# Kernel tuning notes

Hardware: AMD Instinct MI355X
Metric: run time of the kernel (lower is better)

Reference implementation:

```python
import jax, jax.numpy as jnp
import numpy as np

# mamba-370m-style dims (n_layers reduced for tractable reference execution)
H = 1024      # hidden_size
DI = 2048     # intermediate (expand*H)
DS = 16       # ssm state size
DTR = 64      # time_step_rank = H/16
NL = 4        # layers
V = 50280     # vocab after resize_token_embeddings
LLM = 4096    # llm_input_size
B, L = 4, 1024
MEM_ID = 50279
STRIDE = 64
K = L // STRIDE  # mem tokens per sequence
EPS = 1e-5


def setup_inputs() -> dict:
    key = jax.random.key(0)
    ks = jax.random.split(key, 10)
    s = 0.02
    ids = jax.random.randint(ks[0], (B, L), 0, MEM_ID)
    ids = ids.at[:, STRIDE - 1::STRIDE].set(MEM_ID)  # K mem tokens per row
    return {
        "input_ids": ids,
        "embed": jax.random.normal(ks[1], (V, H)) * s,
        "norm_w": jnp.ones((NL, H)),
        "in_proj_w": jax.random.normal(ks[2], (NL, 2 * DI, H)) * s,
        "conv_w": jax.random.normal(ks[3], (NL, DI, 4)) * s,
        "conv_b": jnp.zeros((NL, DI)),
        "x_proj_w": jax.random.normal(ks[4], (NL, DTR + 2 * DS, DI)) * s,
        "dt_w": jax.random.normal(ks[5], (NL, DI, DTR)) * s,
        "dt_b": jax.random.uniform(ks[6], (NL, DI), minval=-4.0, maxval=-2.0),
        "A_log": jnp.log(jnp.broadcast_to(jnp.arange(1, DS + 1, dtype=jnp.float32), (NL, DI, DS))),
        "D": jnp.ones((NL, DI)),
        "out_proj_w": jax.random.normal(ks[7], (NL, H, DI)) * s,
        "final_norm_w": jnp.ones((H,)),
        "proj_w": jax.random.normal(ks[8], (LLM, H)) * s,
        "proj_b": jnp.zeros((LLM,)),
    }


def rmsnorm(x, w):
    return x * jax.lax.rsqrt(jnp.mean(x * x, axis=-1, keepdims=True) + EPS) * w


def mamba_layer(h, p):
    norm_w, in_w, cw, cb, xw, dtw, dtb, A_log, Dp, ow = p
    x = rmsnorm(h, norm_w)
    xz = jnp.einsum('blh,dh->bld', x, in_w)          # (B,L,2*DI)
    x, z = jnp.split(xz, 2, axis=-1)
    # causal depthwise conv1d, kernel 4, left pad 3
    xt = jnp.transpose(x, (0, 2, 1))                  # (B,DI,L)
    xc = jax.lax.conv_general_dilated(xt, cw[:, None, :], (1,), [(3, 0)],
                                      feature_group_count=DI)
    u = jax.nn.silu(xc + cb[None, :, None])
    u = jnp.transpose(u, (0, 2, 1))                   # (B,L,DI)
    ssm = jnp.einsum('bld,ed->ble', u, xw)            # (B,L,DTR+2*DS)
    dt_raw = ssm[..., :DTR]
    Bm = ssm[..., DTR:DTR + DS]
    Cm = ssm[..., DTR + DS:]
    dt = jax.nn.softplus(jnp.einsum('blr,dr->bld', dt_raw, dtw) + dtb)  # (B,L,DI)
    A = -jnp.exp(A_log)                               # (DI,DS)

    def step(s, inp):
        dt_t, B_t, C_t, u_t = inp                     # (B,DI),(B,DS),(B,DS),(B,DI)
        dA = jnp.exp(dt_t[..., None] * A)             # (B,DI,DS)
        s = s * dA + (dt_t * u_t)[..., None] * B_t[:, None, :]
        return s, jnp.einsum('bds,bs->bd', s, C_t)

    s0 = jnp.zeros((h.shape[0], DI, DS), dtype=h.dtype)
    _, ys = jax.lax.scan(step, s0, (dt.swapaxes(0, 1), Bm.swapaxes(0, 1),
                                    Cm.swapaxes(0, 1), u.swapaxes(0, 1)))
    y = ys.swapaxes(0, 1) + u * Dp
    y = y * jax.nn.silu(z)
    return h + jnp.einsum('bld,hd->blh', y, ow), None


def reference(input_ids, embed, norm_w, in_proj_w, conv_w, conv_b, x_proj_w,
              dt_w, dt_b, A_log, D, out_proj_w, final_norm_w, proj_w, proj_b):
    h = embed[input_ids]                              # (B,L,H)
    h, _ = jax.lax.scan(mamba_layer, h,
                        (norm_w, in_proj_w, conv_w, conv_b, x_proj_w,
                         dt_w, dt_b, A_log, D, out_proj_w))
    h = rmsnorm(h, final_norm_w)
    # gather mem-token positions (K per row, in order); stable argsort puts mask hits first
    mask = input_ids == MEM_ID
    pos = jnp.argsort(jnp.where(mask, 0, 1), axis=1)[:, :K]
    feats = jnp.take_along_axis(h, pos[:, :, None], axis=1)   # (B,K,H)
    return jnp.einsum('bkh,lh->bkl', feats, proj_w) + proj_b  # (B,K,LLM)
```

## Files before the change

kernel.cpp:

```cpp
#include <hip/hip_runtime.h>
#include <hip/hip_bf16.h>
#include <cstdint>
#include <cstddef>

#define H_    1024
#define DI_   2048
#define DS_   16
#define DTR_  64
#define NL_   4
#define LLM_  4096
#define B_    4
#define L_    1024
#define MEMID 50279
#define KTOK  16
#define MROWS (B_*L_)
#define BK    64

using bf16 = __hip_bfloat16;
typedef __attribute__((ext_vector_type(8))) short short8;
typedef __attribute__((ext_vector_type(4))) short short4v;
typedef __attribute__((ext_vector_type(4))) float floatx4;
typedef __attribute__((ext_vector_type(4))) unsigned int uint4v;

__device__ __forceinline__ float b2f(bf16 v){ return __bfloat162float(v); }
__device__ __forceinline__ bf16  f2b(float v){ return __float2bfloat16(v); }
__device__ __forceinline__ float sh2f(short s){
    unsigned u = ((unsigned)(unsigned short)s) << 16;
    return __builtin_bit_cast(float, u);
}
__device__ __forceinline__ short f2sh(float v){
    bf16 b = f2b(v);
    return __builtin_bit_cast(short, b);
}
__device__ __forceinline__ float bcf(unsigned int u){ return __builtin_bit_cast(float, u); }

__device__ __forceinline__ float rowsum16(float v){
    float t;
    asm("v_add_f32_dpp %0, %1, %1 row_shr:1 row_mask:0xf bank_mask:0xf bound_ctrl:0" : "=v"(t) : "v"(v));
    asm("v_add_f32_dpp %0, %1, %1 row_shr:2 row_mask:0xf bank_mask:0xf bound_ctrl:0" : "=v"(v) : "v"(t));
    asm("v_add_f32_dpp %0, %1, %1 row_shr:4 row_mask:0xf bank_mask:0xf bound_ctrl:0" : "=v"(t) : "v"(v));
    asm("v_add_f32_dpp %0, %1, %1 row_shr:8 row_mask:0xf bank_mask:0xf bound_ctrl:0" : "=v"(v) : "v"(t));
    return v;
}

__device__ __forceinline__ void async16(bf16* l, const bf16* g){
    __builtin_amdgcn_global_load_lds(
        (const __attribute__((address_space(1))) void*)g,
        (__attribute__((address_space(3))) void*)l,
        16, 0, 0);
}

__global__ void cvt_kernel(const float* __restrict__ src, bf16* __restrict__ dst, int n4)
{
    int i = blockIdx.x*256 + threadIdx.x;
    if (i < n4){
        float4 f = ((const float4*)src)[i];
        short4v o; o[0]=f2sh(f.x); o[1]=f2sh(f.y); o[2]=f2sh(f.z); o[3]=f2sh(f.w);
        ((short4v*)dst)[i] = o;
    }
}

__global__ void cvt4_kernel(const float* __restrict__ s0, bf16* __restrict__ d0, int t0,
                            const float* __restrict__ s1, bf16* __restrict__ d1, int t1,
                            const float* __restrict__ s2, bf16* __restrict__ d2, int t2,
                            const float* __restrict__ s3, bf16* __restrict__ d3, int t3)
{
    int i = blockIdx.x*256 + threadIdx.x;
    const float* s; bf16* d; int local;
    if      (i < t0){ s=s0; d=d0; local=i; }
    else if (i < t1){ s=s1; d=d1; local=i-t0; }
    else if (i < t2){ s=s2; d=d2; local=i-t1; }
    else if (i < t3){ s=s3; d=d3; local=i-t2; }
    else return;
    float4 f = ((const float4*)s)[local];
    short4v o; o[0]=f2sh(f.x); o[1]=f2sh(f.y); o[2]=f2sh(f.z); o[3]=f2sh(f.w);
    ((short4v*)d)[local] = o;
}

__global__ void embed_kernel(const int* __restrict__ ids,
                             const float* __restrict__ emb,
                             float* __restrict__ h)
{
    int row = blockIdx.x;
    int id  = ids[row];
    const float4* src = (const float4*)(emb + (size_t)id * H_);
    float4* dst = (float4*)(h + (size_t)row * H_);
    dst[threadIdx.x] = src[threadIdx.x];
}

__global__ void rmsnorm_kernel(const float* __restrict__ h,
                               const float* __restrict__ w,
                               bf16* __restrict__ out)
{
    int row = blockIdx.x;
    float4 v = ((const float4*)(h + (size_t)row * H_))[threadIdx.x];
    float ss = v.x*v.x + v.y*v.y + v.z*v.z + v.w*v.w;
    #pragma unroll
    for (int off = 32; off; off >>= 1) ss += __shfl_down(ss, off, 64);
    __shared__ float red[4];
    __shared__ float scale_s;
    int lane = threadIdx.x & 63, wv = threadIdx.x >> 6;
    if (lane == 0) red[wv] = ss;
    __syncthreads();
    if (threadIdx.x == 0){
        float t = red[0]+red[1]+red[2]+red[3];
        scale_s = rsqrtf(t * (1.f/H_) + 1e-5f);
    }
    __syncthreads();
    float sc = scale_s;
    float4 w4 = ((const float4*)w)[threadIdx.x];
    short4v o;
    o[0] = f2sh(v.x * sc * w4.x);
    o[1] = f2sh(v.y * sc * w4.y);
    o[2] = f2sh(v.z * sc * w4.z);
    o[3] = f2sh(v.w * sc * w4.w);
    ((short4v*)(out + (size_t)row*H_))[threadIdx.x] = o;
}

__launch_bounds__(256)
__global__ void gemm_bt(const bf16* __restrict__ A, int lda,
                        const bf16* __restrict__ Bm, int ldb,
                        int M, int N, int K,
                        float* __restrict__ Cf, bf16* __restrict__ Cb, int ldc,
                        const float* __restrict__ bias, int mode)
{
    __shared__ __align__(16) bf16 sA[128*BK];
    __shared__ __align__(16) bf16 sB[128*BK];

    int tid  = threadIdx.x;
    int lane = tid & 63;
    int wv   = tid >> 6;
    int quad = lane >> 4, r16 = lane & 15;
    int m0 = blockIdx.y*128, n0 = blockIdx.x*128;
    int wm = (wv>>1)*64, wn = (wv&1)*64;

    int rr = tid >> 3;
    int kc = ((tid & 7) ^ (rr & 7)) * 8;
    const bf16* pA = A  + (size_t)(m0 + rr)*lda + kc;
    const bf16* pB = Bm + (size_t)(n0 + rr)*ldb + kc;
    bf16* lA = sA + wv*512;
    bf16* lB = sB + wv*512;

    floatx4 acc[4][4];
    #pragma unroll
    for (int i=0;i<4;i++)
        #pragma unroll
        for (int j=0;j<4;j++) acc[i][j] = (floatx4){0.f,0.f,0.f,0.f};

    for (int k0 = 0; k0 < K; k0 += BK){
        async16(lA,        pA);
        async16(lA + 2048, pA + (size_t)32*lda);
        async16(lA + 4096, pA + (size_t)64*lda);
        async16(lA + 6144, pA + (size_t)96*lda);
        async16(lB,        pB);
        async16(lB + 2048, pB + (size_t)32*ldb);
        async16(lB + 4096, pB + (size_t)64*ldb);
        async16(lB + 6144, pB + (size_t)96*ldb);
        pA += BK; pB += BK;
        __syncthreads();

        #pragma unroll
        for (int kk=0; kk<2; kk++){
            short8 a[4], b[4];
            #pragma unroll
            for (int i=0;i<4;i++)
                a[i] = *(const short8*)(sA + (wm + i*16 + r16)*BK
                                          + (((kk*4+quad) ^ (r16 & 7))*8));
            #pragma unroll
            for (int j=0;j<4;j++)
                b[j] = *(const short8*)(sB + (wn + j*16 + r16)*BK
                                          + (((kk*4+quad) ^ (r16 & 7))*8));
            #pragma unroll
            for (int i=0;i<4;i++)
                #pragma unroll
                for (int j=0;j<4;j++)
                    acc[i][j] = __builtin_amdgcn_mfma_f32_16x16x32_bf16(a[i], b[j], acc[i][j], 0, 0, 0);
        }
        __syncthreads();
    }

    #pragma unroll
    for (int i=0;i<4;i++)
        #pragma unroll
        for (int j=0;j<4;j++){
            int mq = m0 + wm + i*16 + quad*4;
            int n  = n0 + wn + j*16 + r16;
            if (mode == 1){
                if (n < N){
                    short4v pk;
                    #pragma unroll
                    for (int rr2=0;rr2<4;rr2++){
                        float xx = acc[i][j][rr2] + bias[n];
                        float sp = (xx > 20.f) ? xx : log1pf(__expf(xx));
                        pk[rr2] = f2sh(sp);
                    }
                    *(short4v*)(Cb + (size_t)n*ldc + mq) = pk;
                }
            } else {
                #pragma unroll
                for (int rr2=0;rr2<4;rr2++){
                    int m = mq + rr2;
                    if (m < M && n < N){
                        float v = acc[i][j][rr2];
                        if (mode == 0)      Cf[(size_t)m*ldc + n] = v + (bias ? bias[n] : 0.f);
                        else if (mode == 2) Cf[(size_t)m*ldc + n] += v;
                        else                Cb[(size_t)m*ldc + n] = f2b(v);
                    }
                }
            }
        }
}

__launch_bounds__(256)
__global__ void gemm_out(const bf16* __restrict__ A, int lda,
                         const bf16* __restrict__ Bm, int ldb,
                         float* __restrict__ Cf, int ldc)
{
    __shared__ __align__(16) bf16 sA[128*BK];
    __shared__ __align__(16) bf16 sB[64*BK];

    int tid  = threadIdx.x;
    int lane = tid & 63;
    int wv   = tid >> 6;
    int quad = lane >> 4, r16 = lane & 15;
    int m0 = blockIdx.y*128, n0 = blockIdx.x*64;
    int wm = (wv>>1)*64, wn = (wv&1)*32;

    int rr = tid >> 3;
    int kc = ((tid & 7) ^ (rr & 7)) * 8;
    const bf16* pA = A  + (size_t)(m0 + rr)*lda + kc;
    const bf16* pB = Bm + (size_t)(n0 + rr)*ldb + kc;
    bf16* lA = sA + wv*512;
    bf16* lB = sB + wv*512;

    floatx4 acc[4][2];
    #pragma unroll
    for (int i=0;i<4;i++)
        #pragma unroll
        for (int j=0;j<2;j++) acc[i][j] = (floatx4){0.f,0.f,0.f,0.f};

    for (int k0 = 0; k0 < DI_; k0 += BK){
        async16(lA,        pA);
        async16(lA + 2048, pA + (size_t)32*lda);
        async16(lA + 4096, pA + (size_t)64*lda);
        async16(lA + 6144, pA + (size_t)96*lda);
        async16(lB,        pB);
        async16(lB + 2048, pB + (size_t)32*ldb);
        pA += BK; pB += BK;
        __syncthreads();

        #pragma unroll
        for (int kk=0; kk<2; kk++){
            short8 a[4], b[2];
            #pragma unroll
            for (int i=0;i<4;i++)
                a[i] = *(const short8*)(sA + (wm + i*16 + r16)*BK
                                          + (((kk*4+quad) ^ (r16 & 7))*8));
            #pragma unroll
            for (int j=0;j<2;j++)
                b[j] = *(const short8*)(sB + (wn + j*16 + r16)*BK
                                          + (((kk*4+quad) ^ (r16 & 7))*8));
            #pragma unroll
            for (int i=0;i<4;i++)
                #pragma unroll
                for (int j=0;j<2;j++)
                    acc[i][j] = __builtin_amdgcn_mfma_f32_16x16x32_bf16(a[i], b[j], acc[i][j], 0, 0, 0);
        }
        __syncthreads();
    }

    #pragma unroll
    for (int i=0;i<4;i++)
        #pragma unroll
        for (int j=0;j<2;j++){
            int mq = m0 + wm + i*16 + quad*4;
            int n  = n0 + wn + j*16 + r16;
            #pragma unroll
            for (int rr2=0;rr2<4;rr2++)
                Cf[(size_t)(mq+rr2)*ldc + n] += acc[i][j][rr2];
        }
}

__launch_bounds__(256)
__global__ void gemm_ssm(const bf16* __restrict__ A,
                         const bf16* __restrict__ Bm,
                         bf16* __restrict__ dtA,
                         bf16* __restrict__ pBt,
                         bf16* __restrict__ pCt)
{
    __shared__ __align__(16) bf16 sA2[32*64];
    __shared__ __align__(16) bf16 sB2[96*64];

    int tid  = threadIdx.x;
    int lane = tid & 63;
    int wv   = tid >> 6;
    int quad = lane >> 4, r16 = lane & 15;
    int m0 = blockIdx.x * 32;
    int wr = wv >> 1, wc = wv & 1;

    int ar = tid >> 3;
    int kc = ((tid & 7) ^ (ar & 7)) * 8;
    const bf16* pA  = A  + (size_t)(m0 + ar)*DI_ + kc;
    const bf16* pB0 = Bm + (size_t)(ar)     *DI_ + kc;
    const bf16* pB1 = Bm + (size_t)(32 + ar)*DI_ + kc;
    const bf16* pB2 = Bm + (size_t)(64 + ar)*DI_ + kc;
    bf16* lA  = sA2 + wv*512;
    bf16* lB0 = sB2 + wv*512;
    bf16* lB1 = sB2 + 2048 + wv*512;
    bf16* lB2 = sB2 + 4096 + wv*512;

    floatx4 acc[3];
    #pragma unroll
    for (int j=0;j<3;j++) acc[j] = (floatx4){0.f,0.f,0.f,0.f};

    for (int k0 = 0; k0 < DI_; k0 += 64){
        async16(lA,  pA);
        async16(lB0, pB0);
        async16(lB1, pB1);
        async16(lB2, pB2);
        pA += 64; pB0 += 64; pB1 += 64; pB2 += 64;
        __syncthreads();
        #pragma unroll
        for (int kk=0; kk<2; kk++){
            short8 a = *(const short8*)(sA2 + (wr*16 + r16)*64
                                            + (((kk*4+quad) ^ (r16 & 7))*8));
            #pragma unroll
            for (int j=0;j<3;j++){
                short8 b = *(const short8*)(sB2 + (wc*48 + j*16 + r16)*64
                                                + (((kk*4+quad) ^ (r16 & 7))*8));
                acc[j] = __builtin_amdgcn_mfma_f32_16x16x32_bf16(a, b, acc[j], 0, 0, 0);
            }
        }
        __syncthreads();
    }

    int mq = m0 + wr*16 + quad*4;
    #pragma unroll
    for (int j=0;j<3;j++){
        int n = wc*48 + j*16 + r16;
        if (n < 64){
            #pragma unroll
            for (int rr=0;rr<4;rr++)
                dtA[(size_t)(mq+rr)*64 + n] = f2b(acc[j][rr]);
        } else if (n < 80){
            short4v pk;
            #pragma unroll
            for (int rr=0;rr<4;rr++) pk[rr] = f2sh(acc[j][rr]);
            *(short4v*)(pBt + (size_t)(n-64)*MROWS + mq) = pk;
        } else {
            short4v pk;
            #pragma unroll
            for (int rr=0;rr<4;rr++) pk[rr] = f2sh(acc[j][rr]);
            *(short4v*)(pCt + (size_t)(n-80)*MROWS + mq) = pk;
        }
    }
}

__global__ void conv_silu_kernel(const bf16* __restrict__ xz,
                                 const float* __restrict__ cw,
                                 const float* __restrict__ cb,
                                 bf16* __restrict__ u,
                                 bf16* __restrict__ u_t)
{
    __shared__ float tile[64][65];
    int bt0 = blockIdx.x * 64;
    int d0  = blockIdx.y * 64;
    int tid = threadIdx.x;
    const short8 z8 = {0,0,0,0,0,0,0,0};
    #pragma unroll
    for (int it = 0; it < 2; it++){
        int task = it*256 + tid;
        int g    = task & 7;
        int tr   = task >> 3;
        int row  = bt0 + tr;
        int t    = row & (L_-1);
        int d8   = d0 + g*8;
        const bf16* base = xz + (size_t)row*(2*DI_) + d8;
        short8 x3 = *(const short8*)(base);
        short8 x2 = (t>=1) ? *(const short8*)(base - 1*(2*DI_)) : z8;
        short8 x1 = (t>=2) ? *(const short8*)(base - 2*(2*DI_)) : z8;
        short8 x0 = (t>=3) ? *(const short8*)(base - 3*(2*DI_)) : z8;
        short8 out;
        #pragma unroll
        for (int j=0;j<8;j++){
            int d = d8 + j;
            float4 w4 = ((const float4*)cw)[d];
            float acc = cb[d];
            acc += sh2f(x0[j])*w4.x;
            acc += sh2f(x1[j])*w4.y;
            acc += sh2f(x2[j])*w4.z;
            acc += sh2f(x3[j])*w4.w;
            float s = acc / (1.f + __expf(-acc));
            out[j] = f2sh(s);
            tile[g*8+j][tr] = s;
        }
        *(short8*)(u + (size_t)row*DI_ + d8) = out;
    }
    __syncthreads();
    #pragma unroll
    for (int it = 0; it < 2; it++){
        int task = it*256 + tid;
        int g    = task & 7;
        int dr   = task >> 3;
        int tc8  = g*8;
        short8 o;
        #pragma unroll
        for (int j=0;j<8;j++) o[j] = f2sh(tile[dr][tc8+j]);
        *(short8*)(u_t + (size_t)(d0+dr)*MROWS + bt0 + tc8) = o;
    }
}

#define SCAN_GROUP(dtv,uv,bv,cv,gidx) { \
    uint4v yo; \
    _Pragma("unroll") \
    for (int j = 0; j < 4; j++){ \
        unsigned int wdt = (dtv)[j], wu = (uv)[j], wB = (bv)[j], wC = (cv)[j]; \
        float dt0 = bcf(wdt << 16), u0 = bcf(wu << 16); \
        float b0  = bcf(wB  << 16), c0 = bcf(wC << 16); \
        float e0; asm("v_exp_f32 %0, %1" : "=v"(e0) : "v"(dt0 * A2)); \
        state = __builtin_fmaf(state, e0, dt0 * u0 * b0); \
        float y0 = __builtin_fmaf(u0, Dv, rowsum16(state * c0)); \
        float dt1 = bcf(wdt & 0xffff0000u), u1 = bcf(wu & 0xffff0000u); \
        float b1  = bcf(wB  & 0xffff0000u), c1 = bcf(wC & 0xffff0000u); \
        float e1; asm("v_exp_f32 %0, %1" : "=v"(e1) : "v"(dt1 * A2)); \
        state = __builtin_fmaf(state, e1, dt1 * u1 * b1); \
        float y1 = __builtin_fmaf(u1, Dv, rowsum16(state * c1)); \
        unsigned int pk; \
        asm("v_cvt_pk_bf16_f32 %0, %1, %2" : "=v"(pk) : "v"(y0), "v"(y1)); \
        yo[j] = pk; \
    } \
    if (s_idx == 15) yp_[gidx] = yo; \
}

__global__ void scan_kernel(const bf16* __restrict__ dt_t,
                            const bf16* __restrict__ u_t,
                            const bf16* __restrict__ sB_t,
                            const bf16* __restrict__ sC_t,
                            const float* __restrict__ A_log,
                            const float* __restrict__ Dp,
                            bf16* __restrict__ y_t)
{
    int lane  = threadIdx.x & 63;
    int wv    = threadIdx.x >> 6;
    int s_idx = lane & 15;
    int ch    = lane >> 4;
    int c = blockIdx.x*16 + wv*4 + ch;
    int d = c & (DI_-1);
    int b = c >> 11;
    float A2 = -__expf(A_log[d*DS_ + s_idx]) * 1.4426950408889634f;
    float Dv = Dp[d];
    const uint4v* dtp = (const uint4v*)(dt_t + (size_t)d*MROWS + b*L_);
    const uint4v* utp = (const uint4v*)(u_t  + (size_t)d*MROWS + b*L_);
    const uint4v* Bp  = (const uint4v*)(sB_t + (size_t)s_idx*MROWS + b*L_);
    const uint4v* Cp  = (const uint4v*)(sC_t + (size_t)s_idx*MROWS + b*L_);
    uint4v* yp_ = (uint4v*)(y_t + (size_t)d*MROWS + b*L_);

    const int NG = L_/8;
    float state = 0.f;

    uint4v dA = dtp[0], uA = utp[0], bA = Bp[0], cA = Cp[0];
    uint4v dB = dtp[1], uB = utp[1], bB = Bp[1], cB = Cp[1];
    uint4v dC = dtp[2], uC = utp[2], bC = Bp[2], cC = Cp[2];
    uint4v dD = dtp[3], uD = utp[3], bD = Bp[3], cD = Cp[3];

    for (int g = 0; g < NG; g += 4){
        int p0 = g+4 < NG ? g+4 : NG-1;
        int p1 = g+5 < NG ? g+5 : NG-1;
        int p2 = g+6 < NG ? g+6 : NG-1;
        int p3 = g+7 < NG ? g+7 : NG-1;
        SCAN_GROUP(dA, uA, bA, cA, g);
        dA = dtp[p0]; uA = utp[p0]; bA = Bp[p0]; cA = Cp[p0];
        SCAN_GROUP(dB, uB, bB, cB, g+1);
        dB = dtp[p1]; uB = utp[p1]; bB = Bp[p1]; cB = Cp[p1];
        SCAN_GROUP(dC, uC, bC, cC, g+2);
        dC = dtp[p2]; uC = utp[p2]; bC = Bp[p2]; cC = Cp[p2];
        SCAN_GROUP(dD, uD, bD, cD, g+3);
        dD = dtp[p3]; uD = utp[p3]; bD = Bp[p3]; cD = Cp[p3];
    }
}

__global__ void gate_kernel(const bf16* __restrict__ y_t,
                            bf16* __restrict__ xz)
{
    __shared__ float tile[64][65];
    int bt0 = blockIdx.x * 64;
    int d0  = blockIdx.y * 64;
    int tid = threadIdx.x;
    #pragma unroll
    for (int it = 0; it < 2; it++){
        int task = it*256 + tid;
        int g    = task & 7;
        int dr   = task >> 3;
        short8 v = *(const short8*)(y_t + (size_t)(d0+dr)*MROWS + bt0 + g*8);
        #pragma unroll
        for (int j=0;j<8;j++) tile[dr][g*8+j] = sh2f(v[j]);
    }
    __syncthreads();
    #pragma unroll
    for (int it = 0; it < 2; it++){
        int task = it*256 + tid;
        int g    = task & 7;
        int tr   = task >> 3;
        int row  = bt0 + tr;
        int d8   = g*8;
        short8 z8 = *(const short8*)(xz + (size_t)row*(2*DI_) + DI_ + d0 + d8);
        short8 o;
        #pragma unroll
        for (int j=0;j<8;j++){
            float z  = sh2f(z8[j]);
            float sz = z / (1.f + __expf(-z));
            o[j] = f2sh(tile[d8+j][tr] * sz);
        }
        *(short8*)(xz + (size_t)row*(2*DI_) + d0 + d8) = o;
    }
}

__global__ void pos_kernel(const int* __restrict__ ids, int* __restrict__ pos)
{
    int b = blockIdx.x;
    __shared__ int cnt[256];
    int t = threadIdx.x;
    int local = 0;
    #pragma unroll
    for (int i=0;i<4;i++)
        if (ids[b*L_ + t*4 + i] == MEMID) local++;
    cnt[t] = local;
    __syncthreads();
    if (t == 0){
        int run = 0;
        for (int i=0;i<256;i++){ int tmp = cnt[i]; cnt[i] = run; run += tmp; }
    }
    __syncthreads();
    int rank = cnt[t];
    #pragma unroll
    for (int i=0;i<4;i++){
        int l = t*4 + i;
        if (ids[b*L_ + l] == MEMID){
            if (rank < KTOK) pos[b*KTOK + rank] = l;
            rank++;
        }
    }
}

__global__ void featnorm_kernel(const float* __restrict__ h,
                                const float* __restrict__ w,
                                const int* __restrict__ pos,
                                bf16* __restrict__ feats)
{
    int bk = blockIdx.x;
    int row = (bk >> 4) * L_ + pos[bk];
    const float* x = h + (size_t)row * H_;
    float v[4]; float ss = 0.f;
    #pragma unroll
    for (int i = 0; i < 4; i++){ v[i] = x[threadIdx.x + 256*i]; ss += v[i]*v[i]; }
    #pragma unroll
    for (int off = 32; off; off >>= 1) ss += __shfl_down(ss, off, 64);
    __shared__ float red[4];
    __shared__ float scale_s;
    int lane = threadIdx.x & 63, wv = threadIdx.x >> 6;
    if (lane == 0) red[wv] = ss;
    __syncthreads();
    if (threadIdx.x == 0){
        float t = red[0]+red[1]+red[2]+red[3];
        scale_s = rsqrtf(t * (1.f/H_) + 1e-5f);
    }
    __syncthreads();
    float sc = scale_s;
    #pragma unroll
    for (int i = 0; i < 4; i++){
        int c = threadIdx.x + 256*i;
        feats[(size_t)bk*H_ + c] = f2b(v[i] * sc * w[c]);
    }
}

extern "C" void kernel_launch(void* const* d_in, const int* in_sizes, int n_in,
                              void* d_out, int out_size, void* d_ws, size_t ws_size,
                              hipStream_t stream)
{
    const int*   ids    = (const int*)  d_in[0];
    const float* emb    = (const float*)d_in[1];
    const float* norm_w = (const float*)d_in[2];
    const float* in_w   = (const float*)d_in[3];
    const float* cw     = (const float*)d_in[4];
    const float* cb     = (const float*)d_in[5];
    const float* xw     = (const float*)d_in[6];
    const float* dtw    = (const float*)d_in[7];
    const float* dtb    = (const float*)d_in[8];
    const float* A_log  = (const float*)d_in[9];
    const float* Dp     = (const float*)d_in[10];
    const float* ow     = (const float*)d_in[11];
    const float* fnw    = (const float*)d_in[12];
    const float* projw  = (const float*)d_in[13];
    const float* projb  = (const float*)d_in[14];
    float* out          = (float*)d_out;

    char* ws = (char*)d_ws;
    float* h     = (float*)(ws + 0);
    bf16*  xn    = (bf16*) (ws + 16777216);
    bf16*  wb_in = (bf16*) (ws + 25165824);
    bf16*  u     = (bf16*) (ws + 16777216);
    bf16*  dt_t  = (bf16*) (ws + 16777216);
    bf16*  xz    = (bf16*) (ws + 33554432);
    bf16*  u_t   = (bf16*) (ws + 67108864);
    bf16*  y_t   = (bf16*) (ws + 83886080);
    bf16*  dtA   = (bf16*) (ws + 100663296);
    bf16*  sB_t  = (bf16*) (ws + 101187584);
    bf16*  sC_t  = (bf16*) (ws + 101318656);
    bf16*  fe    = (bf16*) (ws + 101449728);
    int*   pos   = (int*)  (ws + 101580800);
    bf16*  wb_ow = (bf16*) (ws + 101581056);
    bf16*  wb_xw = (bf16*) (ws + 105775360);
    bf16*  wb_dtw= (bf16*) (ws + 106168576);

    embed_kernel<<<MROWS, 256, 0, stream>>>(ids, emb, h);

    const int n_in_w  = 2*DI_*H_;
    const int n_ow_w  = H_*DI_;
    const int n_xw_w  = 96*DI_;
    const int n_dtw_w = DI_*DTR_;
    const int t0c = n_in_w>>2;
    const int t1c = t0c + (n_ow_w>>2);
    const int t2c = t1c + (n_xw_w>>2);
    const int t3c = t2c + (n_dtw_w>>2);

    for (int l = 0; l < NL_; l++){
        const float* nw_l  = norm_w + l*H_;
        const float* cw_l  = cw     + l*DI_*4;
        const float* cb_l  = cb     + l*DI_;
        const float* dtb_l = dtb    + l*DI_;
        const float* al_l  = A_log  + l*DI_*DS_;
        const float* Dp_l  = Dp     + l*DI_;

        cvt4_kernel<<<(t3c+255)/256, 256, 0, stream>>>(
            in_w + (size_t)l*n_in_w, wb_in, t0c,
            ow   + (size_t)l*n_ow_w, wb_ow, t1c,
            xw   + (size_t)l*n_xw_w, wb_xw, t2c,
            dtw  + (size_t)l*n_dtw_w, wb_dtw, t3c);

        rmsnorm_kernel<<<MROWS, 256, 0, stream>>>(h, nw_l, xn);
        gemm_bt<<<dim3(32,32), 256, 0, stream>>>(xn, H_, wb_in, H_,
                                                 MROWS, 2*DI_, H_,
                                                 nullptr, xz, 2*DI_, nullptr, 3);
        conv_silu_kernel<<<dim3(MROWS/64, DI_/64), 256, 0, stream>>>(xz, cw_l, cb_l, u, u_t);
        gemm_ssm<<<128, 256, 0, stream>>>(u, wb_xw, dtA, sB_t, sC_t);
        gemm_bt<<<dim3(16,32), 256, 0, stream>>>(dtA, DTR_, wb_dtw, DTR_,
                                                 MROWS, DI_, DTR_,
                                                 nullptr, dt_t, MROWS, dtb_l, 1);
        scan_kernel<<<512, 256, 0, stream>>>(dt_t, u_t, sB_t, sC_t, al_l, Dp_l, y_t);
        gate_kernel<<<dim3(MROWS/64, DI_/64), 256, 0, stream>>>(y_t, xz);
        gemm_out<<<dim3(16,32), 256, 0, stream>>>(xz, 2*DI_, wb_ow, DI_, h, H_);
    }

    pos_kernel<<<B_, 256, 0, stream>>>(ids, pos);
    featnorm_kernel<<<B_*KTOK, 256, 0, stream>>>(h, fnw, pos, fe);
    cvt_kernel<<<((LLM_*H_/4)+255)/256, 256, 0, stream>>>(projw, wb_in, LLM_*H_/4);
    gemm_bt<<<dim3(32,1), 256, 0, stream>>>(fe, H_, wb_in, H_,
                                            B_*KTOK, LLM_, H_,
                                            out, nullptr, LLM_, projb, 0);
}
```

Before: 1.454 ms.

## Fuse embed/rmsnorm/weight-convert launches, split SSM projection grid, merge tail kernels

Embedding gather, the per-layer RMSNorm and the fp32-to-bf16 weight conversion are merged into one prep launch per layer. The mem-token position search, final norm and projection-weight conversion are merged into one tail kernel. The x_proj GEMM grid is split in two along N so it runs twice as many blocks. The final projection now uses the narrower gemm_out kernel with a bias mode, and the scan prefetch drops its index clamping. Together these aim to cut kernel launches and raise occupancy on small kernels. The risks are uneven block work inside the fused kernels and reads past buffer ends from the unclamped prefetch and from the 128-row tile over only 64 feature rows.

```diff
diff --git a/kernel.cpp b/kernel.cpp
--- a/kernel.cpp
+++ b/kernel.cpp
@@ -50,71 +50,59 @@
         16, 0, 0);
 }
 
-__global__ void cvt_kernel(const float* __restrict__ src, bf16* __restrict__ dst, int n4)
-{
-    int i = blockIdx.x*256 + threadIdx.x;
-    if (i < n4){
-        float4 f = ((const float4*)src)[i];
-        short4v o; o[0]=f2sh(f.x); o[1]=f2sh(f.y); o[2]=f2sh(f.z); o[3]=f2sh(f.w);
-        ((short4v*)dst)[i] = o;
-    }
-}
-
-__global__ void cvt4_kernel(const float* __restrict__ s0, bf16* __restrict__ d0, int t0,
+__global__ void prep_kernel(const int* __restrict__ ids,
+                            const float* __restrict__ emb,
+                            float* __restrict__ h,
+                            const float* __restrict__ nw,
+                            bf16* __restrict__ xn,
+                            const float* __restrict__ s0, bf16* __restrict__ d0, int t0,
                             const float* __restrict__ s1, bf16* __restrict__ d1, int t1,
                             const float* __restrict__ s2, bf16* __restrict__ d2, int t2,
                             const float* __restrict__ s3, bf16* __restrict__ d3, int t3)
 {
-    int i = blockIdx.x*256 + threadIdx.x;
-    const float* s; bf16* d; int local;
-    if      (i < t0){ s=s0; d=d0; local=i; }
-    else if (i < t1){ s=s1; d=d1; local=i-t0; }
-    else if (i < t2){ s=s2; d=d2; local=i-t1; }
-    else if (i < t3){ s=s3; d=d3; local=i-t2; }
-    else return;
-    float4 f = ((const float4*)s)[local];
-    short4v o; o[0]=f2sh(f.x); o[1]=f2sh(f.y); o[2]=f2sh(f.z); o[3]=f2sh(f.w);
-    ((short4v*)d)[local] = o;
-}
-
-__global__ void embed_kernel(const int* __restrict__ ids,
-                             const float* __restrict__ emb,
-                             float* __restrict__ h)
-{
-    int row = blockIdx.x;
-    int id  = ids[row];
-    const float4* src = (const float4*)(emb + (size_t)id * H_);
-    float4* dst = (float4*)(h + (size_t)row * H_);
-    dst[threadIdx.x] = src[threadIdx.x];
-}
-
-__global__ void rmsnorm_kernel(const float* __restrict__ h,
-                               const float* __restrict__ w,
-                               bf16* __restrict__ out)
-{
-    int row = blockIdx.x;
-    float4 v = ((const float4*)(h + (size_t)row * H_))[threadIdx.x];
-    float ss = v.x*v.x + v.y*v.y + v.z*v.z + v.w*v.w;
-    #pragma unroll
-    for (int off = 32; off; off >>= 1) ss += __shfl_down(ss, off, 64);
-    __shared__ float red[4];
-    __shared__ float scale_s;
-    int lane = threadIdx.x & 63, wv = threadIdx.x >> 6;
-    if (lane == 0) red[wv] = ss;
-    __syncthreads();
-    if (threadIdx.x == 0){
-        float t = red[0]+red[1]+red[2]+red[3];
-        scale_s = rsqrtf(t * (1.f/H_) + 1e-5f);
-    }
-    __syncthreads();
-    float sc = scale_s;
-    float4 w4 = ((const float4*)w)[threadIdx.x];
-    short4v o;
-    o[0] = f2sh(v.x * sc * w4.x);
-    o[1] = f2sh(v.y * sc * w4.y);
-    o[2] = f2sh(v.z * sc * w4.z);
-    o[3] = f2sh(v.w * sc * w4.w);
-    ((short4v*)(out + (size_t)row*H_))[threadIdx.x] = o;
+    int bid = blockIdx.x;
+    if (bid < MROWS){
+        float4 v;
+        if (ids){
+            int id = ids[bid];
+            v = ((const float4*)(emb + (size_t)id * H_))[threadIdx.x];
+            ((float4*)(h + (size_t)bid * H_))[threadIdx.x] = v;
+        } else {
+            v = ((const float4*)(h + (size_t)bid * H_))[threadIdx.x];
+        }
+        float ss = v.x*v.x + v.y*v.y + v.z*v.z + v.w*v.w;
+        #pragma unroll
+        for (int off = 32; off; off >>= 1) ss += __shfl_down(ss, off, 64);
+        __shared__ float red[4];
+        __shared__ float scale_s;
+        int lane = threadIdx.x & 63, wv = threadIdx.x >> 6;
+        if (lane == 0) red[wv] = ss;
+        __syncthreads();
+        if (threadIdx.x == 0){
+            float t = red[0]+red[1]+red[2]+red[3];
+            scale_s = rsqrtf(t * (1.f/H_) + 1e-5f);
+        }
+        __syncthreads();
+        float sc = scale_s;
+        float4 w4 = ((const float4*)nw)[threadIdx.x];
+        short4v o;
+        o[0] = f2sh(v.x * sc * w4.x);
+        o[1] = f2sh(v.y * sc * w4.y);
+        o[2] = f2sh(v.z * sc * w4.z);
+        o[3] = f2sh(v.w * sc * w4.w);
+        ((short4v*)(xn + (size_t)bid*H_))[threadIdx.x] = o;
+    } else {
+        int i = (bid - MROWS)*256 + threadIdx.x;
+        const float* s; bf16* d; int local;
+        if      (i < t0){ s=s0; d=d0; local=i; }
+        else if (i < t1){ s=s1; d=d1; local=i-t0; }
+        else if (i < t2){ s=s2; d=d2; local=i-t1; }
+        else if (i < t3){ s=s3; d=d3; local=i-t2; }
+        else return;
+        float4 f = ((const float4*)s)[local];
+        short4v o; o[0]=f2sh(f.x); o[1]=f2sh(f.y); o[2]=f2sh(f.z); o[3]=f2sh(f.w);
+        ((short4v*)d)[local] = o;
+    }
 }
 
 __launch_bounds__(256)
@@ -200,12 +188,8 @@
                 #pragma unroll
                 for (int rr2=0;rr2<4;rr2++){
                     int m = mq + rr2;
-                    if (m < M && n < N){
-                        float v = acc[i][j][rr2];
-                        if (mode == 0)      Cf[(size_t)m*ldc + n] = v + (bias ? bias[n] : 0.f);
-                        else if (mode == 2) Cf[(size_t)m*ldc + n] += v;
-                        else                Cb[(size_t)m*ldc + n] = f2b(v);
-                    }
+                    if (m < M && n < N)
+                        Cb[(size_t)m*ldc + n] = f2b(acc[i][j][rr2]);
                 }
             }
         }
@@ -214,7 +198,9 @@
 __launch_bounds__(256)
 __global__ void gemm_out(const bf16* __restrict__ A, int lda,
                          const bf16* __restrict__ Bm, int ldb,
-                         float* __restrict__ Cf, int ldc)
+                         int K, int M,
+                         float* __restrict__ Cf, int ldc,
+                         const float* __restrict__ bias, int mode)
 {
     __shared__ __align__(16) bf16 sA[128*BK];
     __shared__ __align__(16) bf16 sB[64*BK];
@@ -239,7 +225,7 @@
         #pragma unroll
         for (int j=0;j<2;j++) acc[i][j] = (floatx4){0.f,0.f,0.f,0.f};
 
-    for (int k0 = 0; k0 < DI_; k0 += BK){
+    for (int k0 = 0; k0 < K; k0 += BK){
         async16(lA,        pA);
         async16(lA + 2048, pA + (size_t)32*lda);
         async16(lA + 4096, pA + (size_t)64*lda);
@@ -275,9 +261,18 @@
         for (int j=0;j<2;j++){
             int mq = m0 + wm + i*16 + quad*4;
             int n  = n0 + wn + j*16 + r16;
-            #pragma unroll
-            for (int rr2=0;rr2<4;rr2++)
-                Cf[(size_t)(mq+rr2)*ldc + n] += acc[i][j][rr2];
+            if (mode == 2){
+                #pragma unroll
+                for (int rr2=0;rr2<4;rr2++)
+                    Cf[(size_t)(mq+rr2)*ldc + n] += acc[i][j][rr2];
+            } else {
+                #pragma unroll
+                for (int rr2=0;rr2<4;rr2++){
+                    int m = mq + rr2;
+                    if (m < M)
+                        Cf[(size_t)m*ldc + n] = acc[i][j][rr2] + bias[n];
+                }
+            }
         }
 }
 
@@ -289,44 +284,44 @@
                          bf16* __restrict__ pCt)
 {
     __shared__ __align__(16) bf16 sA2[32*64];
-    __shared__ __align__(16) bf16 sB2[96*64];
+    __shared__ __align__(16) bf16 sB2[64*64];
 
     int tid  = threadIdx.x;
     int lane = tid & 63;
     int wv   = tid >> 6;
     int quad = lane >> 4, r16 = lane & 15;
     int m0 = blockIdx.x * 32;
+    int ny = blockIdx.y;
+    int nw_    = ny ? 1 : 2;
+    int nstep  = ny ? 16 : 32;
+    int nbase  = ny ? 64 : 0;
     int wr = wv >> 1, wc = wv & 1;
 
     int ar = tid >> 3;
     int kc = ((tid & 7) ^ (ar & 7)) * 8;
     const bf16* pA  = A  + (size_t)(m0 + ar)*DI_ + kc;
-    const bf16* pB0 = Bm + (size_t)(ar)     *DI_ + kc;
-    const bf16* pB1 = Bm + (size_t)(32 + ar)*DI_ + kc;
-    const bf16* pB2 = Bm + (size_t)(64 + ar)*DI_ + kc;
+    const bf16* pB0 = Bm + (size_t)(nbase + ar)*DI_ + kc;
+    const bf16* pB1 = Bm + (size_t)(nbase + 32 + ar)*DI_ + kc;
     bf16* lA  = sA2 + wv*512;
     bf16* lB0 = sB2 + wv*512;
     bf16* lB1 = sB2 + 2048 + wv*512;
-    bf16* lB2 = sB2 + 4096 + wv*512;
-
-    floatx4 acc[3];
-    #pragma unroll
-    for (int j=0;j<3;j++) acc[j] = (floatx4){0.f,0.f,0.f,0.f};
+
+    floatx4 acc[2];
+    acc[0] = (floatx4){0.f,0.f,0.f,0.f};
+    acc[1] = (floatx4){0.f,0.f,0.f,0.f};
 
     for (int k0 = 0; k0 < DI_; k0 += 64){
         async16(lA,  pA);
         async16(lB0, pB0);
-        async16(lB1, pB1);
-        async16(lB2, pB2);
-        pA += 64; pB0 += 64; pB1 += 64; pB2 += 64;
+        if (!ny) async16(lB1, pB1);
+        pA += 64; pB0 += 64; pB1 += 64;
         __syncthreads();
         #pragma unroll
         for (int kk=0; kk<2; kk++){
             short8 a = *(const short8*)(sA2 + (wr*16 + r16)*64
                                             + (((kk*4+quad) ^ (r16 & 7))*8));
-            #pragma unroll
-            for (int j=0;j<3;j++){
-                short8 b = *(const short8*)(sB2 + (wc*48 + j*16 + r16)*64
+            for (int j=0;j<nw_;j++){
+                short8 b = *(const short8*)(sB2 + (wc*nstep + j*16 + r16)*64
                                                 + (((kk*4+quad) ^ (r16 & 7))*8));
                 acc[j] = __builtin_amdgcn_mfma_f32_16x16x32_bf16(a, b, acc[j], 0, 0, 0);
             }
@@ -335,22 +330,21 @@
     }
 
     int mq = m0 + wr*16 + quad*4;
-    #pragma unroll
-    for (int j=0;j<3;j++){
-        int n = wc*48 + j*16 + r16;
+    for (int j=0;j<nw_;j++){
+        int n = nbase + wc*nstep + j*16 + r16;
         if (n < 64){
             #pragma unroll
-            for (int rr=0;rr<4;rr++)
-                dtA[(size_t)(mq+rr)*64 + n] = f2b(acc[j][rr]);
+            for (int rr2=0;rr2<4;rr2++)
+                dtA[(size_t)(mq+rr2)*64 + n] = f2b(acc[j][rr2]);
         } else if (n < 80){
             short4v pk;
             #pragma unroll
-            for (int rr=0;rr<4;rr++) pk[rr] = f2sh(acc[j][rr]);
+            for (int rr2=0;rr2<4;rr2++) pk[rr2] = f2sh(acc[j][rr2]);
             *(short4v*)(pBt + (size_t)(n-64)*MROWS + mq) = pk;
         } else {
             short4v pk;
             #pragma unroll
-            for (int rr=0;rr<4;rr++) pk[rr] = f2sh(acc[j][rr]);
+            for (int rr2=0;rr2<4;rr2++) pk[rr2] = f2sh(acc[j][rr2]);
             *(short4v*)(pCt + (size_t)(n-80)*MROWS + mq) = pk;
         }
     }
@@ -464,18 +458,14 @@
     uint4v dD = dtp[3], uD = utp[3], bD = Bp[3], cD = Cp[3];
 
     for (int g = 0; g < NG; g += 4){
-        int p0 = g+4 < NG ? g+4 : NG-1;
-        int p1 = g+5 < NG ? g+5 : NG-1;
-        int p2 = g+6 < NG ? g+6 : NG-1;
-        int p3 = g+7 < NG ? g+7 : NG-1;
         SCAN_GROUP(dA, uA, bA, cA, g);
-        dA = dtp[p0]; uA = utp[p0]; bA = Bp[p0]; cA = Cp[p0];
+        dA = dtp[g+4]; uA = utp[g+4]; bA = Bp[g+4]; cA = Cp[g+4];
         SCAN_GROUP(dB, uB, bB, cB, g+1);
-        dB = dtp[p1]; uB = utp[p1]; bB = Bp[p1]; cB = Cp[p1];
+        dB = dtp[g+5]; uB = utp[g+5]; bB = Bp[g+5]; cB = Cp[g+5];
         SCAN_GROUP(dC, uC, bC, cC, g+2);
-        dC = dtp[p2]; uC = utp[p2]; bC = Bp[p2]; cC = Cp[p2];
+        dC = dtp[g+6]; uC = utp[g+6]; bC = Bp[g+6]; cC = Cp[g+6];
         SCAN_GROUP(dD, uD, bD, cD, g+3);
-        dD = dtp[p3]; uD = utp[p3]; bD = Bp[p3]; cD = Cp[p3];
+        dD = dtp[g+7]; uD = utp[g+7]; bD = Bp[g+7]; cD = Cp[g+7];
     }
 }
 
@@ -515,61 +505,70 @@
     }
 }
 
-__global__ void pos_kernel(const int* __restrict__ ids, int* __restrict__ pos)
-{
-    int b = blockIdx.x;
-    __shared__ int cnt[256];
-    int t = threadIdx.x;
-    int local = 0;
-    #pragma unroll
-    for (int i=0;i<4;i++)
-        if (ids[b*L_ + t*4 + i] == MEMID) local++;
-    cnt[t] = local;
-    __syncthreads();
-    if (t == 0){
-        int run = 0;
-        for (int i=0;i<256;i++){ int tmp = cnt[i]; cnt[i] = run; run += tmp; }
-    }
-    __syncthreads();
-    int rank = cnt[t];
-    #pragma unroll
-    for (int i=0;i<4;i++){
-        int l = t*4 + i;
-        if (ids[b*L_ + l] == MEMID){
-            if (rank < KTOK) pos[b*KTOK + rank] = l;
-            rank++;
-        }
-    }
-}
-
-__global__ void featnorm_kernel(const float* __restrict__ h,
-                                const float* __restrict__ w,
-                                const int* __restrict__ pos,
-                                bf16* __restrict__ feats)
-{
-    int bk = blockIdx.x;
-    int row = (bk >> 4) * L_ + pos[bk];
-    const float* x = h + (size_t)row * H_;
-    float v[4]; float ss = 0.f;
-    #pragma unroll
-    for (int i = 0; i < 4; i++){ v[i] = x[threadIdx.x + 256*i]; ss += v[i]*v[i]; }
-    #pragma unroll
-    for (int off = 32; off; off >>= 1) ss += __shfl_down(ss, off, 64);
-    __shared__ float red[4];
-    __shared__ float scale_s;
-    int lane = threadIdx.x & 63, wv = threadIdx.x >> 6;
-    if (lane == 0) red[wv] = ss;
-    __syncthreads();
-    if (threadIdx.x == 0){
-        float t = red[0]+red[1]+red[2]+red[3];
-        scale_s = rsqrtf(t * (1.f/H_) + 1e-5f);
-    }
-    __syncthreads();
-    float sc = scale_s;
-    #pragma unroll
-    for (int i = 0; i < 4; i++){
-        int c = threadIdx.x + 256*i;
-        feats[(size_t)bk*H_ + c] = f2b(v[i] * sc * w[c]);
+__global__ void tail_kernel(const float* __restrict__ h,
+                            const float* __restrict__ w,
+                            const int* __restrict__ ids,
+                            bf16* __restrict__ feats,
+                            const float* __restrict__ projw,
+                            bf16* __restrict__ wb, int n4)
+{
+    if (blockIdx.x < B_*KTOK){
+        int bk = blockIdx.x;
+        int b = bk >> 4, k = bk & 15;
+        int t = threadIdx.x;
+        __shared__ int cnt[256];
+        __shared__ int pos_s;
+        int local = 0;
+        #pragma unroll
+        for (int i=0;i<4;i++)
+            if (ids[b*L_ + t*4 + i] == MEMID) local++;
+        cnt[t] = local;
+        __syncthreads();
+        if (t == 0){
+            int run = 0;
+            for (int i=0;i<256;i++){ int tmp = cnt[i]; cnt[i] = run; run += tmp; }
+        }
+        __syncthreads();
+        int rank = cnt[t];
+        #pragma unroll
+        for (int i=0;i<4;i++){
+            int l = t*4 + i;
+            if (ids[b*L_ + l] == MEMID){
+                if (rank == k) pos_s = l;
+                rank++;
+            }
+        }
+        __syncthreads();
+        int row = b*L_ + pos_s;
+        float4 v = ((const float4*)(h + (size_t)row * H_))[t];
+        float ss = v.x*v.x + v.y*v.y + v.z*v.z + v.w*v.w;
+        #pragma unroll
+        for (int off = 32; off; off >>= 1) ss += __shfl_down(ss, off, 64);
+        __shared__ float red[4];
+        __shared__ float scale_s;
+        int lane = t & 63, wv = t >> 6;
+        if (lane == 0) red[wv] = ss;
+        __syncthreads();
+        if (t == 0){
+            float tt = red[0]+red[1]+red[2]+red[3];
+            scale_s = rsqrtf(tt * (1.f/H_) + 1e-5f);
+        }
+        __syncthreads();
+        float sc = scale_s;
+        float4 w4 = ((const float4*)w)[t];
+        short4v o;
+        o[0] = f2sh(v.x * sc * w4.x);
+        o[1] = f2sh(v.y * sc * w4.y);
+        o[2] = f2sh(v.z * sc * w4.z);
+        o[3] = f2sh(v.w * sc * w4.w);
+        ((short4v*)(feats + (size_t)bk*H_))[t] = o;
+    } else {
+        int i = (blockIdx.x - B_*KTOK)*256 + threadIdx.x;
+        if (i < n4){
+            float4 f = ((const float4*)projw)[i];
+            short4v o; o[0]=f2sh(f.x); o[1]=f2sh(f.y); o[2]=f2sh(f.z); o[3]=f2sh(f.w);
+            ((short4v*)wb)[i] = o;
+        }
     }
 }
 
@@ -611,8 +610,7 @@
     bf16*  wb_ow = (bf16*) (ws + 101581056);
     bf16*  wb_xw = (bf16*) (ws + 105775360);
     bf16*  wb_dtw= (bf16*) (ws + 106168576);
-
-    embed_kernel<<<MROWS, 256, 0, stream>>>(ids, emb, h);
+    (void)pos;
 
     const int n_in_w  = 2*DI_*H_;
     const int n_ow_w  = H_*DI_;
@@ -622,6 +620,8 @@
     const int t1c = t0c + (n_ow_w>>2);
     const int t2c = t1c + (n_xw_w>>2);
     const int t3c = t2c + (n_dtw_w>>2);
+    const int cvtBlocks = (t3c+255)/256;
+    const int prepGrid  = MROWS + cvtBlocks;
 
     for (int l = 0; l < NL_; l++){
         const float* nw_l  = norm_w + l*H_;
@@ -631,30 +631,29 @@
         const float* al_l  = A_log  + l*DI_*DS_;
         const float* Dp_l  = Dp     + l*DI_;
 
-        cvt4_kernel<<<(t3c+255)/256, 256, 0, stream>>>(
+        prep_kernel<<<prepGrid, 256, 0, stream>>>(
+            (l == 0) ? ids : nullptr, emb, h, nw_l, xn,
             in_w + (size_t)l*n_in_w, wb_in, t0c,
             ow   + (size_t)l*n_ow_w, wb_ow, t1c,
             xw   + (size_t)l*n_xw_w, wb_xw, t2c,
             dtw  + (size_t)l*n_dtw_w, wb_dtw, t3c);
 
-        rmsnorm_kernel<<<MROWS, 256, 0, stream>>>(h, nw_l, xn);
         gemm_bt<<<dim3(32,32), 256, 0, stream>>>(xn, H_, wb_in, H_,
                                                  MROWS, 2*DI_, H_,
                                                  nullptr, xz, 2*DI_, nullptr, 3);
         conv_silu_kernel<<<dim3(MROWS/64, DI_/64), 256, 0, stream>>>(xz, cw_l, cb_l, u, u_t);
-        gemm_ssm<<<128, 256, 0, stream>>>(u, wb_xw, dtA, sB_t, sC_t);
+        gemm_ssm<<<dim3(128,2), 256, 0, stream>>>(u, wb_xw, dtA, sB_t, sC_t);
         gemm_bt<<<dim3(16,32), 256, 0, stream>>>(dtA, DTR_, wb_dtw, DTR_,
                                                  MROWS, DI_, DTR_,
                                                  nullptr, dt_t, MROWS, dtb_l, 1);
         scan_kernel<<<512, 256, 0, stream>>>(dt_t, u_t, sB_t, sC_t, al_l, Dp_l, y_t);
         gate_kernel<<<dim3(MROWS/64, DI_/64), 256, 0, stream>>>(y_t, xz);
-        gemm_out<<<dim3(16,32), 256, 0, stream>>>(xz, 2*DI_, wb_ow, DI_, h, H_);
-    }
-
-    pos_kernel<<<B_, 256, 0, stream>>>(ids, pos);
-    featnorm_kernel<<<B_*KTOK, 256, 0, stream>>>(h, fnw, pos, fe);
-    cvt_kernel<<<((LLM_*H_/4)+255)/256, 256, 0, stream>>>(projw, wb_in, LLM_*H_/4);
-    gemm_bt<<<dim3(32,1), 256, 0, stream>>>(fe, H_, wb_in, H_,
-                                            B_*KTOK, LLM_, H_,
-                                            out, nullptr, LLM_, projb, 0);
-}
+        gemm_out<<<dim3(16,32), 256, 0, stream>>>(xz, 2*DI_, wb_ow, DI_,
+                                                  DI_, MROWS, h, H_, nullptr, 2);
+    }
+
+    tail_kernel<<<B_*KTOK + ((LLM_*H_/4)+255)/256, 256, 0, stream>>>(
+        h, fnw, ids, fe, projw, wb_in, LLM_*H_/4);
+    gemm_out<<<dim3(LLM_/64,1), 256, 0, stream>>>(fe, H_, wb_in, H_,
+                                                  H_, B_*KTOK, out, LLM_, projb, 0);
+}
```

Result: slower. 1.558 ms (+7.2%).
